# Performance work log

Hardware: AMD Instinct MI355X
Metric: run time of the kernel (lower is better)

## Reference

```python
import jax, jax.numpy as jnp
import numpy as np

NEG_SLOPE = 0.2  # PyG GATConv default negative_slope


def gat_conv(x, src, dst, W, a_src, a_dst, b, concat):
    """One PyG-style GATConv (eval mode, self-loops already added to src/dst).
    x: [N, Fin], W: [Fin, H*C], a_src/a_dst: [H, C], b: [H*C] or [C].
    """
    N = x.shape[0]
    H, C = a_src.shape
    h = (x @ W).reshape(N, H, C)                       # [N,H,C]
    alpha_s = jnp.sum(h * a_src, axis=-1)              # [N,H]
    alpha_d = jnp.sum(h * a_dst, axis=-1)              # [N,H]
    e = alpha_s[src] + alpha_d[dst]                    # [E,H]
    e = jax.nn.leaky_relu(e, NEG_SLOPE)
    # scatter-softmax over incoming edges of each destination node
    m = jax.ops.segment_max(e, dst, num_segments=N)    # [N,H]
    p = jnp.exp(e - m[dst])                            # [E,H]
    s = jax.ops.segment_sum(p, dst, num_segments=N)    # [N,H]
    alpha = p / s[dst]                                 # [E,H]
    msg = h[src] * alpha[:, :, None]                   # [E,H,C]
    out = jax.ops.segment_sum(msg, dst, num_segments=N)  # [N,H,C]
    out = out.reshape(N, H * C) if concat else out.mean(axis=1)
    return out + b


def setup_inputs() -> dict:
    key = jax.random.key(0)
    ks = jax.random.split(key, 12)
    N, E = 50000, 800000
    IN_C, HID, HEADS, OUT_C = 1, 32, 4, 1
    HW = HID * HEADS  # 128
    x = jax.random.normal(ks[0], (N, IN_C), dtype=jnp.float32)
    edge_index = jax.random.randint(ks[1], (2, E), 0, N, dtype=jnp.int64)
    g = 0.1
    inp = {
        "x": x,
        "edge_index": edge_index,
        "W1": jax.random.normal(ks[2], (IN_C, HW), dtype=jnp.float32) * g,
        "a_src1": jax.random.normal(ks[3], (HEADS, HID), dtype=jnp.float32) * g,
        "a_dst1": jax.random.normal(ks[4], (HEADS, HID), dtype=jnp.float32) * g,
        "b1": jnp.zeros((HW,), dtype=jnp.float32),
        "W2": jax.random.normal(ks[5], (HW, HW), dtype=jnp.float32) * g,
        "a_src2": jax.random.normal(ks[6], (HEADS, HID), dtype=jnp.float32) * g,
        "a_dst2": jax.random.normal(ks[7], (HEADS, HID), dtype=jnp.float32) * g,
        "b2": jnp.zeros((HW,), dtype=jnp.float32),
        "W3": jax.random.normal(ks[8], (HW, OUT_C), dtype=jnp.float32) * g,
        "a_src3": jax.random.normal(ks[9], (1, OUT_C), dtype=jnp.float32) * g,
        "a_dst3": jax.random.normal(ks[10], (1, OUT_C), dtype=jnp.float32) * g,
        "b3": jnp.zeros((OUT_C,), dtype=jnp.float32),
    }
    return inp


def reference(x, edge_index, W1, a_src1, a_dst1, b1, W2, a_src2, a_dst2, b2,
              W3, a_src3, a_dst3, b3):
    N = x.shape[0]
    loop = jnp.arange(N, dtype=edge_index.dtype)
    # PyG GATConv add_self_loops=True (each layer): add once, reused by all layers
    src = jnp.concatenate([edge_index[0], loop])
    dst = jnp.concatenate([edge_index[1], loop])
    h = gat_conv(x, src, dst, W1, a_src1, a_dst1, b1, concat=True)
    h = jax.nn.elu(h)  # dropout is identity in eval mode
    h = gat_conv(h, src, dst, W2, a_src2, a_dst2, b2, concat=True)
    h = jax.nn.elu(h)
    out = gat_conv(h, src, dst, W3, a_src3, a_dst3, b3, concat=False)
    return out
```

## Files before the change

kernel.cpp:

```cpp
#include <hip/hip_runtime.h>
#include <math.h>

#define NEG_SLOPE 0.2f

typedef _Float16 hv4 __attribute__((ext_vector_type(4)));
typedef _Float16 hv8 __attribute__((ext_vector_type(8)));

static __device__ __forceinline__ float leaky(float v){ return v > 0.f ? v : NEG_SLOPE * v; }
static __device__ __forceinline__ float eluf(float v){ return v > 0.f ? v : expm1f(v); }
static __device__ __forceinline__ float eluf_fast(float v){ return v > 0.f ? v : __expf(v) - 1.f; }

__global__ void __launch_bounds__(256) hist_k(const int* __restrict__ edst, int* __restrict__ deg,
                                              int Eg, int Etot, int N){
  const int slot = blockIdx.x & 7;
  const int lo = (int)(((long long)slot * N) >> 3);
  const int hi = (int)(((long long)(slot + 1) * N) >> 3);
  const int stride = (gridDim.x >> 3) * blockDim.x;
  for (int e = (blockIdx.x >> 3) * blockDim.x + threadIdx.x; e < Etot; e += stride){
    int d = (e < Eg) ? edst[e] : (e - Eg);
    if (d >= lo && d < hi) atomicAdd(&deg[d], 1);
  }
}

__global__ void __launch_bounds__(256) scatter_k(const int* __restrict__ esrc, const int* __restrict__ edst,
                                                 int* __restrict__ cursor, int* __restrict__ csr_src,
                                                 int Eg, int Etot, int N){
  const int slot = blockIdx.x & 7;
  const int lo = (int)(((long long)slot * N) >> 3);
  const int hi = (int)(((long long)(slot + 1) * N) >> 3);
  const int stride = (gridDim.x >> 3) * blockDim.x;
  for (int e = (blockIdx.x >> 3) * blockDim.x + threadIdx.x; e < Etot; e += stride){
    int s, d;
    if (e < Eg){ d = edst[e]; if (d < lo || d >= hi) continue; s = esrc[e]; }
    else { s = d = e - Eg; if (d < lo || d >= hi) continue; }
    int pos = atomicAdd(&cursor[d], 1);
    csr_src[pos] = s;
  }
}

__global__ void __launch_bounds__(256) scan_part_k(const int* __restrict__ deg,
                                                   int* __restrict__ bsum, int N){
  __shared__ int red[256];
  const int t = threadIdx.x;
  const int base = blockIdx.x * 2048;
  int sum = 0;
  #pragma unroll
  for (int i = 0; i < 8; ++i){
    int idx = base + t + i * 256;
    if (idx < N) sum += deg[idx];
  }
  red[t] = sum; __syncthreads();
  #pragma unroll
  for (int d = 128; d; d >>= 1){
    if (t < d) red[t] += red[t + d];
    __syncthreads();
  }
  if (t == 0) bsum[blockIdx.x] = red[0];
}

__global__ void scan_tops_k(const int* __restrict__ bsum, int* __restrict__ boff,
                            int* __restrict__ row, int nb, int N){
  int t = threadIdx.x;
  int v = (t < nb) ? bsum[t] : 0;
  int orig = v;
  #pragma unroll
  for (int off = 1; off < 64; off <<= 1){
    int u = __shfl_up(v, off, 64);
    if (t >= off) v += u;
  }
  if (t < nb) boff[t] = v - orig;
  if (t == nb - 1) row[N] = v;
}

__global__ void __launch_bounds__(256) scan_write_k(const int* __restrict__ deg,
                                                    const int* __restrict__ boff,
                                                    int* __restrict__ row, int* __restrict__ cursor, int N){
  __shared__ int sdeg[2048];
  __shared__ int tsum[256];
  const int t = threadIdx.x;
  const int base = blockIdx.x * 2048;
  for (int i = t; i < 2048; i += 256){
    int idx = base + i;
    sdeg[i] = (idx < N) ? deg[idx] : 0;
  }
  __syncthreads();
  const int off = t * 8;
  int sum = 0;
  #pragma unroll
  for (int i = 0; i < 8; ++i) sum += sdeg[off + i];
  tsum[t] = sum; __syncthreads();
  for (int d = 1; d < 256; d <<= 1){
    int v = (t >= d) ? tsum[t - d] : 0;
    __syncthreads();
    tsum[t] += v;
    __syncthreads();
  }
  int run = boff[blockIdx.x] + ((t == 0) ? 0 : tsum[t - 1]);
  #pragma unroll
  for (int i = 0; i < 8; ++i){
    int idx = base + off + i;
    if (idx < N){ row[idx] = run; cursor[idx] = run; run += sdeg[off + i]; }
  }
}

__global__ void dots1_k(const float* __restrict__ W1, const float* __restrict__ a_s,
                        const float* __restrict__ a_d, float* __restrict__ dAdD){
  int t = threadIdx.x;
  float ps = W1[t] * a_s[t];
  float pd = W1[t] * a_d[t];
  #pragma unroll
  for (int off = 16; off; off >>= 1){
    ps += __shfl_xor(ps, off, 32);
    pd += __shfl_xor(pd, off, 32);
  }
  if ((t & 31) == 0){ dAdD[t >> 5] = ps; dAdD[4 + (t >> 5)] = pd; }
}

__global__ void __launch_bounds__(256) r1_k(const int* __restrict__ row, const int* __restrict__ csr_src,
                                            const float* __restrict__ x, const float* __restrict__ dAdD,
                                            float4* __restrict__ r4, int N){
  int node = blockIdx.x * 32 + (threadIdx.x >> 3);
  if (node >= N) return;
  const int q = threadIdx.x & 7;
  const int start = row[node], end = row[node + 1];
  const float xd = x[node];
  float dA0 = dAdD[0], dA1 = dAdD[1], dA2 = dAdD[2], dA3 = dAdD[3];
  float e0d = xd * dAdD[4], e1d = xd * dAdD[5], e2d = xd * dAdD[6], e3d = xd * dAdD[7];

  float s0 = 0.f, s1 = 0.f, s2 = 0.f, s3 = 0.f;
  float t0 = 0.f, t1 = 0.f, t2 = 0.f, t3 = 0.f;
  for (int i = start + q; i < end; i += 8){
    float xs = x[csr_src[i]];
    float p0 = __expf(leaky(xs * dA0 + e0d));
    float p1 = __expf(leaky(xs * dA1 + e1d));
    float p2 = __expf(leaky(xs * dA2 + e2d));
    float p3 = __expf(leaky(xs * dA3 + e3d));
    s0 += p0; s1 += p1; s2 += p2; s3 += p3;
    t0 += p0 * xs; t1 += p1 * xs; t2 += p2 * xs; t3 += p3 * xs;
  }
  #pragma unroll
  for (int off = 4; off; off >>= 1){
    s0 += __shfl_xor(s0, off, 8); t0 += __shfl_xor(t0, off, 8);
    s1 += __shfl_xor(s1, off, 8); t1 += __shfl_xor(t1, off, 8);
    s2 += __shfl_xor(s2, off, 8); t2 += __shfl_xor(t2, off, 8);
    s3 += __shfl_xor(s3, off, 8); t3 += __shfl_xor(t3, off, 8);
  }
  if (q == 0) r4[node] = make_float4(t0 / s0, t1 / s1, t2 / s2, t3 / s3);
}

__global__ void __launch_bounds__(256) gemm2_k(const float4* __restrict__ r4,
                                               const float* __restrict__ W1f, const float* __restrict__ b1f,
                                               const float* __restrict__ W,
                                               const float* __restrict__ a_s, const float* __restrict__ a_d,
                                               _Float16* __restrict__ hh, float* __restrict__ as_, float* __restrict__ ad_,
                                               int N){
  __shared__ float sA[128][68];
  __shared__ _Float16 sW[2][16][128];
  const int t = threadIdx.x;
  const int n0 = blockIdx.x * 64;
  const int tx = t & 15, ty = t >> 4;
  const int c0 = tx * 8, r0 = ty * 4;

  const int wk = t >> 5;
  const int wq = t & 31;

  float4 rw0, rw1;
  auto gloadW = [&](int k0){
    rw0 = *(const float4*)&W[(size_t)(k0 + wk) * 128 + wq * 4];
    rw1 = *(const float4*)&W[(size_t)(k0 + wk + 8) * 128 + wq * 4];
  };
  auto sstoreW = [&](int buf){
    hv4 a = {(_Float16)rw0.x, (_Float16)rw0.y, (_Float16)rw0.z, (_Float16)rw0.w};
    hv4 b = {(_Float16)rw1.x, (_Float16)rw1.y, (_Float16)rw1.z, (_Float16)rw1.w};
    *(hv4*)&sW[buf][wk][wq * 4]     = a;
    *(hv4*)&sW[buf][wk + 8][wq * 4] = b;
  };

  {
    const int nl = t & 63, q = t >> 6;
    const int gn = n0 + nl;
    float r = 0.f;
    const bool valid = (gn < N);
    if (valid){
      float4 rv = r4[gn];
      r = (q == 0) ? rv.x : (q == 1) ? rv.y : (q == 2) ? rv.z : rv.w;
    }
    #pragma unroll
    for (int j = 0; j < 32; ++j){
      const int c = q * 32 + j;
      float v = W1f[c] * r + b1f[c];
      v = eluf_fast(v);
      sA[c][nl] = valid ? v : 0.f;
    }
  }

  float acc[4][8];
  #pragma unroll
  for (int r = 0; r < 4; ++r)
    #pragma unroll
    for (int c = 0; c < 8; ++c) acc[r][c] = 0.f;

  gloadW(0); sstoreW(0); __syncthreads();

  #pragma unroll 1
  for (int tile = 0; tile < 8; ++tile){
    const int buf = tile & 1;
    if (tile < 7) gloadW((tile + 1) * 16);
    #pragma unroll
    for (int k = 0; k < 16; ++k){
      float4 aa = *(const float4*)&sA[tile * 16 + k][r0];
      hv8 wh = *(const hv8*)&sW[buf][k][c0];
      float av[4] = {aa.x, aa.y, aa.z, aa.w};
      float wv[8];
      #pragma unroll
      for (int c = 0; c < 8; ++c) wv[c] = (float)wh[c];
      #pragma unroll
      for (int r = 0; r < 4; ++r)
        #pragma unroll
        for (int c = 0; c < 8; ++c) acc[r][c] += av[r] * wv[c];
    }
    if (tile < 7){ sstoreW(1 - buf); __syncthreads(); }
  }

  float asv[8], adv[8];
  #pragma unroll
  for (int c = 0; c < 8; ++c){ asv[c] = a_s[c0 + c]; adv[c] = a_d[c0 + c]; }

  const int hd  = tx >> 2;
  const int off = (tx & 3) * 8;

  #pragma unroll
  for (int r = 0; r < 4; ++r){
    int n = n0 + r0 + r;
    if (n >= N) continue;
    hv8 hv;
    #pragma unroll
    for (int c = 0; c < 8; ++c) hv[c] = (_Float16)acc[r][c];
    *(hv8*)&hh[((size_t)hd * N + n) * 32 + off] = hv;
    float ps = 0.f, pd = 0.f;
    #pragma unroll
    for (int c = 0; c < 8; ++c){ ps += acc[r][c] * asv[c]; pd += acc[r][c] * adv[c]; }
    ps += __shfl_xor(ps, 1); ps += __shfl_xor(ps, 2);
    pd += __shfl_xor(pd, 1); pd += __shfl_xor(pd, 2);
    if ((tx & 3) == 0){
      as_[(size_t)hd * N + n] = ps;
      ad_[(size_t)hd * N + n] = pd;
    }
  }
}

__global__ void __launch_bounds__(256) node_aggr2_k(const int* __restrict__ row, const int* __restrict__ csr_src,
                                                    const float* __restrict__ as_, const float* __restrict__ ad_,
                                                    const _Float16* __restrict__ hh, const float* __restrict__ b2,
                                                    const float* __restrict__ W3, float* __restrict__ h3, int N){
  const int slot   = blockIdx.x & 7;
  const int chunk  = blockIdx.x >> 3;
  const int head   = slot >> 1;
  const int parity = slot & 1;
  const int t  = threadIdx.x;
  const int nl = t >> 2;
  const int q  = t & 3;
  const int node = chunk * 128 + parity * 64 + nl;
  if (node >= N) return;
  const int start = row[node], end = row[node + 1];
  const float* __restrict__ ash = as_ + (size_t)head * N;
  const _Float16* __restrict__ hhh = hh + (size_t)head * N * 32 + q * 8;
  const float adv = ad_[(size_t)head * N + node];

  float s = 0.f;
  float acc[8] = {0.f, 0.f, 0.f, 0.f, 0.f, 0.f, 0.f, 0.f};
  int i = start;

  int pre = (4 - (start & 3)) & 3;
  if (pre > end - start) pre = end - start;
  for (int k = 0; k < pre; ++k, ++i){
    int src = csr_src[i];
    float p = __expf(leaky(ash[src] + adv));
    hv8 hv = *(const hv8*)&hhh[(size_t)src * 32];
    s += p;
    #pragma unroll
    for (int c = 0; c < 8; ++c) acc[c] += (float)hv[c] * p;
  }
  for (; i + 4 <= end; i += 4){
    int4 ia = *(const int4*)&csr_src[i];
    float a0 = ash[ia.x], a1 = ash[ia.y], a2 = ash[ia.z], a3 = ash[ia.w];
    hv8 h0 = *(const hv8*)&hhh[(size_t)ia.x * 32];
    hv8 h1 = *(const hv8*)&hhh[(size_t)ia.y * 32];
    hv8 h2 = *(const hv8*)&hhh[(size_t)ia.z * 32];
    hv8 h3v = *(const hv8*)&hhh[(size_t)ia.w * 32];
    float p0 = __expf(leaky(a0 + adv));
    float p1 = __expf(leaky(a1 + adv));
    float p2 = __expf(leaky(a2 + adv));
    float p3 = __expf(leaky(a3 + adv));
    s += (p0 + p1) + (p2 + p3);
    #pragma unroll
    for (int c = 0; c < 8; ++c)
      acc[c] += (float)h0[c]*p0 + (float)h1[c]*p1 + (float)h2[c]*p2 + (float)h3v[c]*p3;
  }
  for (; i < end; ++i){
    int src = csr_src[i];
    float p = __expf(leaky(ash[src] + adv));
    hv8 hv = *(const hv8*)&hhh[(size_t)src * 32];
    s += p;
    #pragma unroll
    for (int c = 0; c < 8; ++c) acc[c] += (float)hv[c] * p;
  }

  const float inv = 1.f / s;
  const int c0 = head * 32 + q * 8;
  float part = 0.f;
  #pragma unroll
  for (int c = 0; c < 8; ++c){
    float v = eluf(acc[c] * inv + b2[c0 + c]);
    part += v * W3[c0 + c];
  }
  part += __shfl_xor(part, 1, 4);
  part += __shfl_xor(part, 2, 4);
  if (q == 0) unsafeAtomicAdd(&h3[node], part);
}

__global__ void __launch_bounds__(256) node_aggr3_k(const int* __restrict__ row, const int* __restrict__ csr_src,
                                                    const float* __restrict__ h3,
                                                    const float* __restrict__ a_s3, const float* __restrict__ a_d3,
                                                    const float* __restrict__ b3,
                                                    float* __restrict__ out, int N){
  int node = blockIdx.x * 32 + (threadIdx.x >> 3);
  if (node >= N) return;
  int q = threadIdx.x & 7;
  int start = row[node], end = row[node + 1];
  const float a_s3v = a_s3[0];
  const float adv = a_d3[0] * h3[node];
  float s = 0.f, acc = 0.f;
  for (int i = start + q; i < end; i += 8){
    int src = csr_src[i];
    float hv = h3[src];
    float p = __expf(leaky(a_s3v * hv + adv));
    s += p; acc += hv * p;
  }
  #pragma unroll
  for (int off = 4; off; off >>= 1){
    s += __shfl_xor(s, off, 8);
    acc += __shfl_xor(acc, off, 8);
  }
  if (q == 0) out[node] = acc / s + b3[0];
}

extern "C" void kernel_launch(void* const* d_in, const int* in_sizes, int n_in,
                              void* d_out, int out_size, void* d_ws, size_t ws_size,
                              hipStream_t stream){
  const float* x   = (const float*)d_in[0];
  const int*   ei  = (const int*)  d_in[1];
  const float* W1  = (const float*)d_in[2];
  const float* as1 = (const float*)d_in[3];
  const float* ad1 = (const float*)d_in[4];
  const float* b1  = (const float*)d_in[5];
  const float* W2  = (const float*)d_in[6];
  const float* as2 = (const float*)d_in[7];
  const float* ad2 = (const float*)d_in[8];
  const float* b2  = (const float*)d_in[9];
  const float* W3  = (const float*)d_in[10];
  const float* as3 = (const float*)d_in[11];
  const float* ad3 = (const float*)d_in[12];
  const float* b3  = (const float*)d_in[13];

  const int N    = in_sizes[0];
  const int Eg   = in_sizes[1] / 2;
  const int Etot = Eg + N;
  const int* esrc = ei;
  const int* edst = ei + Eg;

  char* w = (char*)d_ws;
  auto carve = [&](size_t bytes)->char*{
    char* p = w; w += (bytes + 15) & ~size_t(15); return p;
  };
  _Float16* hbuf = (_Float16*)carve((size_t)N * 128 * 2);
  float* r4b    = (float*)carve((size_t)N * 4 * 4);
  float* asb    = (float*)carve((size_t)N * 4 * 4);
  float* adb    = (float*)carve((size_t)N * 4 * 4);
  float* h3b    = (float*)carve((size_t)N * 4);
  int*   deg    = (int*)  carve((size_t)N * 4);
  int*   rowp   = (int*)  carve((size_t)(N + 1) * 4);
  int*   cursor = (int*)  carve((size_t)N * 4);
  int*   csr_src= (int*)  carve((size_t)Etot * 4);
  float* dAdD   = (float*)carve(8 * 4);
  int*   bsum   = (int*)  carve(64 * 4);
  int*   boff   = (int*)  carve(64 * 4);

  const int B = 256;
  auto cdiv = [](int a, int b){ return (a + b - 1) / b; };
  const int nb = cdiv(N, 2048);

  hipMemsetAsync(deg, 0, (size_t)N * 4, stream);
  hipMemsetAsync(h3b, 0, (size_t)N * 4, stream);
  hist_k<<<128 * 8, B, 0, stream>>>(edst, deg, Eg, Etot, N);
  scan_part_k<<<nb, B, 0, stream>>>(deg, bsum, N);
  scan_tops_k<<<1, 64, 0, stream>>>(bsum, boff, rowp, nb, N);
  scan_write_k<<<nb, B, 0, stream>>>(deg, boff, rowp, cursor, N);
  scatter_k<<<128 * 8, B, 0, stream>>>(esrc, edst, cursor, csr_src, Eg, Etot, N);

  dots1_k<<<1, 128, 0, stream>>>(W1, as1, ad1, dAdD);
  r1_k<<<cdiv(N, 32), B, 0, stream>>>(rowp, csr_src, x, dAdD, (float4*)r4b, N);

  gemm2_k<<<cdiv(N, 64), B, 0, stream>>>((const float4*)r4b, W1, b1,
                                         W2, as2, ad2, hbuf, asb, adb, N);
  node_aggr2_k<<<cdiv(N, 128) * 8, B, 0, stream>>>(rowp, csr_src, asb, adb,
                                                   hbuf, b2, W3, h3b, N);

  node_aggr3_k<<<cdiv(N, 32), B, 0, stream>>>(rowp, csr_src, h3b, as3, ad3, b3, (float*)d_out, N);
}
```

Baseline: 275.4 us.

## Precompute per-edge attention weights in a separate kernel before layer-2 aggregation

Adds a CSR-order destination array during scatter and a new kernel that computes exp(leaky(as+ad)) for every edge and head into a buffer. The layer-2 aggregation then reads these weights with coalesced loads instead of gathering source scores and recomputing exponentials redundantly across the four lanes per node. In exchange it adds an extra kernel launch, an extra edge-sized write in scatter, and a multi-megabyte intermediate written and read through memory.

```diff
diff --git a/kernel.cpp b/kernel.cpp
--- a/kernel.cpp
+++ b/kernel.cpp
@@ -24,6 +24,7 @@
 
 __global__ void __launch_bounds__(256) scatter_k(const int* __restrict__ esrc, const int* __restrict__ edst,
                                                  int* __restrict__ cursor, int* __restrict__ csr_src,
+                                                 int* __restrict__ csr_dst,
                                                  int Eg, int Etot, int N){
   const int slot = blockIdx.x & 7;
   const int lo = (int)(((long long)slot * N) >> 3);
@@ -35,6 +36,7 @@
     else { s = d = e - Eg; if (d < lo || d >= hi) continue; }
     int pos = atomicAdd(&cursor[d], 1);
     csr_src[pos] = s;
+    csr_dst[pos] = d;
   }
 }
 
@@ -249,10 +251,24 @@
   }
 }
 
+__global__ void __launch_bounds__(256) pk_k(const int* __restrict__ csr_src, const int* __restrict__ csr_dst,
+                                            const float* __restrict__ as_, const float* __restrict__ ad_,
+                                            float* __restrict__ p4, int Etot, int Ep, int N){
+  int i = blockIdx.x * blockDim.x + threadIdx.x;
+  if (i >= Etot) return;
+  int s = csr_src[i], d = csr_dst[i];
+  #pragma unroll
+  for (int h = 0; h < 4; ++h){
+    float e = leaky(as_[(size_t)h * N + s] + ad_[(size_t)h * N + d]);
+    p4[(size_t)h * Ep + i] = __expf(e);
+  }
+}
+
 __global__ void __launch_bounds__(256) node_aggr2_k(const int* __restrict__ row, const int* __restrict__ csr_src,
-                                                    const float* __restrict__ as_, const float* __restrict__ ad_,
+                                                    const float* __restrict__ p4,
                                                     const _Float16* __restrict__ hh, const float* __restrict__ b2,
-                                                    const float* __restrict__ W3, float* __restrict__ h3, int N){
+                                                    const float* __restrict__ W3, float* __restrict__ h3,
+                                                    int N, int Ep){
   const int slot   = blockIdx.x & 7;
   const int chunk  = blockIdx.x >> 3;
   const int head   = slot >> 1;
@@ -263,9 +279,8 @@
   const int node = chunk * 128 + parity * 64 + nl;
   if (node >= N) return;
   const int start = row[node], end = row[node + 1];
-  const float* __restrict__ ash = as_ + (size_t)head * N;
+  const float* __restrict__ ph = p4 + (size_t)head * Ep;
   const _Float16* __restrict__ hhh = hh + (size_t)head * N * 32 + q * 8;
-  const float adv = ad_[(size_t)head * N + node];
 
   float s = 0.f;
   float acc[8] = {0.f, 0.f, 0.f, 0.f, 0.f, 0.f, 0.f, 0.f};
@@ -275,7 +290,7 @@
   if (pre > end - start) pre = end - start;
   for (int k = 0; k < pre; ++k, ++i){
     int src = csr_src[i];
-    float p = __expf(leaky(ash[src] + adv));
+    float p = ph[i];
     hv8 hv = *(const hv8*)&hhh[(size_t)src * 32];
     s += p;
     #pragma unroll
@@ -283,23 +298,19 @@
   }
   for (; i + 4 <= end; i += 4){
     int4 ia = *(const int4*)&csr_src[i];
-    float a0 = ash[ia.x], a1 = ash[ia.y], a2 = ash[ia.z], a3 = ash[ia.w];
+    float4 pv = *(const float4*)&ph[i];
     hv8 h0 = *(const hv8*)&hhh[(size_t)ia.x * 32];
     hv8 h1 = *(const hv8*)&hhh[(size_t)ia.y * 32];
     hv8 h2 = *(const hv8*)&hhh[(size_t)ia.z * 32];
     hv8 h3v = *(const hv8*)&hhh[(size_t)ia.w * 32];
-    float p0 = __expf(leaky(a0 + adv));
-    float p1 = __expf(leaky(a1 + adv));
-    float p2 = __expf(leaky(a2 + adv));
-    float p3 = __expf(leaky(a3 + adv));
-    s += (p0 + p1) + (p2 + p3);
+    s += (pv.x + pv.y) + (pv.z + pv.w);
     #pragma unroll
     for (int c = 0; c < 8; ++c)
-      acc[c] += (float)h0[c]*p0 + (float)h1[c]*p1 + (float)h2[c]*p2 + (float)h3v[c]*p3;
+      acc[c] += (float)h0[c]*pv.x + (float)h1[c]*pv.y + (float)h2[c]*pv.z + (float)h3v[c]*pv.w;
   }
   for (; i < end; ++i){
     int src = csr_src[i];
-    float p = __expf(leaky(ash[src] + adv));
+    float p = ph[i];
     hv8 hv = *(const hv8*)&hhh[(size_t)src * 32];
     s += p;
     #pragma unroll
@@ -366,6 +377,7 @@
   const int N    = in_sizes[0];
   const int Eg   = in_sizes[1] / 2;
   const int Etot = Eg + N;
+  const int Ep   = (Etot + 3) & ~3;
   const int* esrc = ei;
   const int* edst = ei + Eg;
 
@@ -378,10 +390,12 @@
   float* asb    = (float*)carve((size_t)N * 4 * 4);
   float* adb    = (float*)carve((size_t)N * 4 * 4);
   float* h3b    = (float*)carve((size_t)N * 4);
+  float* p4b    = (float*)carve((size_t)Ep * 4 * 4);
   int*   deg    = (int*)  carve((size_t)N * 4);
   int*   rowp   = (int*)  carve((size_t)(N + 1) * 4);
   int*   cursor = (int*)  carve((size_t)N * 4);
   int*   csr_src= (int*)  carve((size_t)Etot * 4);
+  int*   csr_dst= (int*)  carve((size_t)Etot * 4);
   float* dAdD   = (float*)carve(8 * 4);
   int*   bsum   = (int*)  carve(64 * 4);
   int*   boff   = (int*)  carve(64 * 4);
@@ -396,15 +410,16 @@
   scan_part_k<<<nb, B, 0, stream>>>(deg, bsum, N);
   scan_tops_k<<<1, 64, 0, stream>>>(bsum, boff, rowp, nb, N);
   scan_write_k<<<nb, B, 0, stream>>>(deg, boff, rowp, cursor, N);
-  scatter_k<<<128 * 8, B, 0, stream>>>(esrc, edst, cursor, csr_src, Eg, Etot, N);
+  scatter_k<<<128 * 8, B, 0, stream>>>(esrc, edst, cursor, csr_src, csr_dst, Eg, Etot, N);
 
   dots1_k<<<1, 128, 0, stream>>>(W1, as1, ad1, dAdD);
   r1_k<<<cdiv(N, 32), B, 0, stream>>>(rowp, csr_src, x, dAdD, (float4*)r4b, N);
 
   gemm2_k<<<cdiv(N, 64), B, 0, stream>>>((const float4*)r4b, W1, b1,
                                          W2, as2, ad2, hbuf, asb, adb, N);
-  node_aggr2_k<<<cdiv(N, 128) * 8, B, 0, stream>>>(rowp, csr_src, asb, adb,
-                                                   hbuf, b2, W3, h3b, N);
+  pk_k<<<cdiv(Etot, B), B, 0, stream>>>(csr_src, csr_dst, asb, adb, p4b, Etot, Ep, N);
+  node_aggr2_k<<<cdiv(N, 128) * 8, B, 0, stream>>>(rowp, csr_src, p4b,
+                                                   hbuf, b2, W3, h3b, N, Ep);
 
   node_aggr3_k<<<cdiv(N, 32), B, 0, stream>>>(rowp, csr_src, h3b, as3, ad3, b3, (float*)d_out, N);
 }
```

New measurement: 290.2 us. 5.4% more time.
